# Optimization experiments

Measured on AMD Instinct MI355X. Metric: run time of the kernel, lower is better.

## Reference

```python
import jax, jax.numpy as jnp
import numpy as np

IM_H = 256.0
IM_W = 256.0


def setup_inputs() -> dict:
    key = jax.random.key(0)
    k1, k2 = jax.random.split(key)
    feats = jax.random.normal(k1, (8, 64, 64, 64), dtype=jnp.float32)
    Kcam = jax.random.normal(k2, (2, 4, 3, 4), dtype=jnp.float32)
    vmax = jnp.ones((2, 3), dtype=jnp.float32)
    vmin = jnp.zeros((2, 3), dtype=jnp.float32)
    return {"feats": feats, "Kcam": Kcam, "vmax": vmax, "vmin": vmin, "nvox": 48}


def reference(feats, Kcam, vmax, vmin, nvox):
    nR, fdim, fh, fw = feats.shape
    batch, view = Kcam.shape[0], Kcam.shape[1]
    rsz_h = float(fh) / IM_H
    rsz_w = float(fw) / IM_W

    # Build voxel grid per batch: linspace(vmin, vmax, nvox) along each axis.
    t = jnp.linspace(0.0, 1.0, nvox, dtype=jnp.float32)  # [nvox]
    rng = vmin[:, :, None] + (vmax - vmin)[:, :, None] * t  # [batch, 3, nvox]
    shp = (batch, nvox, nvox, nvox)
    gx = jnp.broadcast_to(rng[:, 0, :, None, None], shp)  # meshgrid 'ij' (torch default)
    gy = jnp.broadcast_to(rng[:, 1, None, :, None], shp)
    gz = jnp.broadcast_to(rng[:, 2, None, None, :], shp)
    grid = jnp.stack([gx, gy, gz], axis=1).reshape(batch, 3, -1)  # [batch, 3, nV]
    nV = grid.shape[2]
    rs_grid = jnp.concatenate([grid, jnp.ones((batch, 1, nV), jnp.float32)], axis=1)  # [batch, 4, nV]

    # Perspective projection: [batch, view*3, 4] @ [batch, 4, nV]
    im_p = jnp.einsum('bvrk,bkn->bvrn', Kcam, rs_grid).reshape(batch * view, 3, nV)
    im_x, im_y, im_z = im_p[:, 0, :], im_p[:, 1, :], im_p[:, 2, :]
    im_x = jnp.clip(im_x / im_z * rsz_w, 0.0, fw - 1)
    im_y = jnp.clip(im_y / im_z * rsz_h, 0.0, fh - 1)

    im_x0 = jnp.floor(im_x)
    im_x1 = jnp.clip(im_x0 + 1.0, 0.0, fw - 1)
    im_y0 = jnp.floor(im_y)
    im_y1 = jnp.clip(im_y0 + 1.0, 0.0, fh - 1)

    flat = feats.reshape(nR, fdim, fh * fw)  # [nR, fdim, fh*fw]

    def gather(xi, yi):
        idx = (yi * fw + xi).astype(jnp.int32)  # [nR, nV]
        return jax.vmap(lambda f, i: f[:, i])(flat, idx)  # [nR, fdim, nV]

    Ia = gather(im_x0, im_y0)
    Ib = gather(im_x0, im_y1)
    Ic = gather(im_x1, im_y0)
    Id = gather(im_x1, im_y1)

    wa = ((im_x1 - im_x) * (im_y1 - im_y))[:, None, :]
    wb = ((im_x1 - im_x) * (im_y - im_y0))[:, None, :]
    wc = ((im_x - im_x0) * (im_y1 - im_y))[:, None, :]
    wd = ((im_x - im_x0) * (im_y - im_y0))[:, None, :]

    Ibilin = wa * Ia + wb * Ib + wc * Ic + wd * Id  # [nR, fdim, nV]
    return Ibilin.reshape(nR, fdim, nvox, nvox, nvox)
```

## Files before the change

### kernel.cpp

```cpp
#include <hip/hip_runtime.h>


#define NR    8
#define FDIM  64
#define FH    64
#define FW    64
#define IMG   (FH * FW)
#define NVOX  48
#define NV    (NVOX * NVOX * NVOX)
#define THREADS 256
#define QUARTERS 4
#define VPB   (NV / QUARTERS)
#define ITERS (VPB / THREADS)
#define ROWS  64
#define RS    66

typedef float f32x4 __attribute__((ext_vector_type(4)));
typedef float f32x2 __attribute__((ext_vector_type(2)));

__device__ __forceinline__ int swz(int y, int x) {
    const int g = ((x >> 2) ^ (y & 15));
    return y * RS + (g << 2) + (x & 3);
}

__global__ __launch_bounds__(THREADS, 4) void proj_splat_kernel(
    const float* __restrict__ feats,
    const float* __restrict__ Kcam,
    const float* __restrict__ vmax,
    const float* __restrict__ vmin,
    float* __restrict__ out)
{
    __shared__ f32x2 lds2[ROWS * RS];

    const int t  = threadIdx.x;
    const int cp = blockIdx.x;
    const int qq = blockIdx.y;
    const int r  = blockIdx.z;
    const int b  = r >> 2;

    const float* c0 = feats + ((size_t)r * FDIM + 2 * cp) * IMG;
    const float* c1 = c0 + IMG;
    float* ldsf = reinterpret_cast<float*>(lds2);
#pragma unroll
    for (int p = 0; p < 4; ++p) {
        const int i = p * 1024 + t * 4;
        const int y = i >> 6;
        const int x = i & 63;
        const f32x4 a = *reinterpret_cast<const f32x4*>(c0 + i);
        const f32x4 bb = *reinterpret_cast<const f32x4*>(c1 + i);
        const int fb = 2 * swz(y, x);
        f32x4 s0 = { a.x, bb.x, a.y, bb.y };
        f32x4 s1 = { a.z, bb.z, a.w, bb.w };
        *reinterpret_cast<f32x4*>(ldsf + fb)     = s0;
        *reinterpret_cast<f32x4*>(ldsf + fb + 4) = s1;
    }
    __syncthreads();

    const float inv = 1.0f / (float)(NVOX - 1);
    const float* vmn = vmin + b * 3;
    const float* vmx = vmax + b * 3;
    const float ax = (vmx[0] - vmn[0]) * inv;
    const float ay = (vmx[1] - vmn[1]) * inv;
    const float az = (vmx[2] - vmn[2]) * inv;
    const float* K = Kcam + r * 12;
    const float A0 = K[0] * ax, B0 = K[1] * ay, D0 = K[2]  * az;
    const float C0 = K[0] * vmn[0] + K[1] * vmn[1] + K[2]  * vmn[2] + K[3];
    const float A1 = K[4] * ax, B1 = K[5] * ay, D1 = K[6]  * az;
    const float C1 = K[4] * vmn[0] + K[5] * vmn[1] + K[6]  * vmn[2] + K[7];
    const float A2 = K[8] * ax, B2 = K[9] * ay, D2 = K[10] * az;
    const float C2 = K[8] * vmn[0] + K[9] * vmn[1] + K[10] * vmn[2] + K[11];

    float* o0 = out + ((size_t)r * FDIM + 2 * cp) * NV;
    float* o1 = o0 + NV;

    int n = qq * VPB + t;
    int i = n / (NVOX * NVOX);
    int j = (n / NVOX) % NVOX;
    int k = n % NVOX;

    for (int it = 0; it < ITERS; ++it) {
        const float fi = (float)i, fj = (float)j, fk = (float)k;
        const float px = C0 + A0 * fi + B0 * fj + D0 * fk;
        const float py = C1 + A1 * fi + B1 * fj + D1 * fk;
        const float pz = C2 + A2 * fi + B2 * fj + D2 * fk;

        const float rz = 0.25f / pz;
        float imx = px * rz;
        float imy = py * rz;
        imx = fminf(fmaxf(imx, 0.0f), (float)(FW - 1));
        imy = fminf(fmaxf(imy, 0.0f), (float)(FH - 1));

        const float x0 = floorf(imx);
        const float x1 = fminf(x0 + 1.0f, (float)(FW - 1));
        const float y0 = floorf(imy);
        const float y1 = fminf(y0 + 1.0f, (float)(FH - 1));

        const float wa = (x1 - imx) * (y1 - imy);
        const float wc = (imx - x0) * (y1 - imy);
        const float wb = (x1 - imx) * (imy - y0);
        const float wd = (imx - x0) * (imy - y0);

        const int ix0 = (int)x0, ix1 = (int)x1;
        const int iy0 = (int)y0, iy1 = (int)y1;

        const f32x2 p00 = lds2[swz(iy0, ix0)];
        const f32x2 p01 = lds2[swz(iy0, ix1)];
        const f32x2 p10 = lds2[swz(iy1, ix0)];
        const f32x2 p11 = lds2[swz(iy1, ix1)];

        const float res0 = wa * p00.x + wc * p01.x + wb * p10.x + wd * p11.x;
        const float res1 = wa * p00.y + wc * p01.y + wb * p10.y + wd * p11.y;
        __builtin_nontemporal_store(res0, o0 + n);
        __builtin_nontemporal_store(res1, o1 + n);

        n += THREADS;
        k += 16;
        if (k >= NVOX) { k -= NVOX; j += 6; } else { j += 5; }
        if (j >= NVOX) { j -= NVOX; i += 1; }
    }
}

extern "C" void kernel_launch(void* const* d_in, const int* in_sizes, int n_in,
                              void* d_out, int out_size, void* d_ws, size_t ws_size,
                              hipStream_t stream) {
    const float* feats = (const float*)d_in[0];
    const float* Kcam  = (const float*)d_in[1];
    const float* vmax  = (const float*)d_in[2];
    const float* vmin  = (const float*)d_in[3];
    float* out = (float*)d_out;

    dim3 grid(FDIM / 2, QUARTERS, NR);
    dim3 block(THREADS);
    proj_splat_kernel<<<grid, block, 0, stream>>>(feats, Kcam, vmax, vmin, out);
}
```

Baseline: 254.6 us.

## Store features as fp16 in LDS, process two voxels per thread, split grid into octants

Feature tiles are converted to half2 and kept in shared memory with an XOR swizzle, which halves the LDS footprint so more blocks fit per CU (launch bounds raised to 8). Each thread now handles two adjacent voxels, advancing the projection incrementally, and writes them with a 2-wide vector store instead of nontemporal scalar stores. The reciprocal becomes a fast approximate rcp, and the grid is split into 8 voxel chunks instead of 4. The fp16 storage and approximate reciprocal reduce numerical precision and may exceed the output tolerance.

```diff
diff --git a/kernel.cpp b/kernel.cpp
--- a/kernel.cpp
+++ b/kernel.cpp
@@ -1,4 +1,5 @@
 #include <hip/hip_runtime.h>
+#include <hip/hip_fp16.h>
 
 
 #define NR    8
@@ -9,50 +10,43 @@
 #define NVOX  48
 #define NV    (NVOX * NVOX * NVOX)
 #define THREADS 256
-#define QUARTERS 4
-#define VPB   (NV / QUARTERS)
-#define ITERS (VPB / THREADS)
-#define ROWS  64
-#define RS    66
+#define OCTS  8
+#define VPB   (NV / OCTS)
+#define ITERS (VPB / (THREADS * 2))
 
 typedef float f32x4 __attribute__((ext_vector_type(4)));
 typedef float f32x2 __attribute__((ext_vector_type(2)));
 
-__device__ __forceinline__ int swz(int y, int x) {
-    const int g = ((x >> 2) ^ (y & 15));
-    return y * RS + (g << 2) + (x & 3);
+__device__ __forceinline__ int slotof(int y, int x) {
+    return (y << 6) + (x ^ (y & 31));
 }
 
-__global__ __launch_bounds__(THREADS, 4) void proj_splat_kernel(
+__global__ __launch_bounds__(THREADS, 8) void proj_splat_kernel(
     const float* __restrict__ feats,
     const float* __restrict__ Kcam,
     const float* __restrict__ vmax,
     const float* __restrict__ vmin,
     float* __restrict__ out)
 {
-    __shared__ f32x2 lds2[ROWS * RS];
+    __shared__ __half2 ldsh[IMG];
 
-    const int t  = threadIdx.x;
-    const int cp = blockIdx.x;
-    const int qq = blockIdx.y;
-    const int r  = blockIdx.z;
-    const int b  = r >> 2;
+    const int t   = threadIdx.x;
+    const int cp  = blockIdx.x;
+    const int oct = blockIdx.y;
+    const int r   = blockIdx.z;
+    const int b   = r >> 2;
 
     const float* c0 = feats + ((size_t)r * FDIM + 2 * cp) * IMG;
     const float* c1 = c0 + IMG;
-    float* ldsf = reinterpret_cast<float*>(lds2);
 #pragma unroll
-    for (int p = 0; p < 4; ++p) {
-        const int i = p * 1024 + t * 4;
-        const int y = i >> 6;
-        const int x = i & 63;
-        const f32x4 a = *reinterpret_cast<const f32x4*>(c0 + i);
-        const f32x4 bb = *reinterpret_cast<const f32x4*>(c1 + i);
-        const int fb = 2 * swz(y, x);
-        f32x4 s0 = { a.x, bb.x, a.y, bb.y };
-        f32x4 s1 = { a.z, bb.z, a.w, bb.w };
-        *reinterpret_cast<f32x4*>(ldsf + fb)     = s0;
-        *reinterpret_cast<f32x4*>(ldsf + fb + 4) = s1;
+    for (int q = 0; q < 4; ++q) {
+        const int idx = q * 1024 + t * 4;
+        const int y = idx >> 6, x = idx & 63;
+        const f32x4 a  = *reinterpret_cast<const f32x4*>(c0 + idx);
+        const f32x4 bb = *reinterpret_cast<const f32x4*>(c1 + idx);
+#pragma unroll
+        for (int m = 0; m < 4; ++m)
+            ldsh[slotof(y, x + m)] = __floats2half2_rn(a[m], bb[m]);
     }
     __syncthreads();
 
@@ -73,49 +67,58 @@
     float* o0 = out + ((size_t)r * FDIM + 2 * cp) * NV;
     float* o1 = o0 + NV;
 
-    int n = qq * VPB + t;
+    int n = oct * VPB + 2 * t;
     int i = n / (NVOX * NVOX);
     int j = (n / NVOX) % NVOX;
     int k = n % NVOX;
 
     for (int it = 0; it < ITERS; ++it) {
         const float fi = (float)i, fj = (float)j, fk = (float)k;
-        const float px = C0 + A0 * fi + B0 * fj + D0 * fk;
-        const float py = C1 + A1 * fi + B1 * fj + D1 * fk;
-        const float pz = C2 + A2 * fi + B2 * fj + D2 * fk;
+        float px = C0 + A0 * fi + B0 * fj + D0 * fk;
+        float py = C1 + A1 * fi + B1 * fj + D1 * fk;
+        float pz = C2 + A2 * fi + B2 * fj + D2 * fk;
 
-        const float rz = 0.25f / pz;
-        float imx = px * rz;
-        float imy = py * rz;
-        imx = fminf(fmaxf(imx, 0.0f), (float)(FW - 1));
-        imy = fminf(fmaxf(imy, 0.0f), (float)(FH - 1));
+        float r0[2], r1[2];
+#pragma unroll
+        for (int v = 0; v < 2; ++v) {
+            const float rz = __builtin_amdgcn_rcpf(pz) * 0.25f;
+            float imx = px * rz;
+            float imy = py * rz;
+            imx = fminf(fmaxf(imx, 0.0f), (float)(FW - 1));
+            imy = fminf(fmaxf(imy, 0.0f), (float)(FH - 1));
 
-        const float x0 = floorf(imx);
-        const float x1 = fminf(x0 + 1.0f, (float)(FW - 1));
-        const float y0 = floorf(imy);
-        const float y1 = fminf(y0 + 1.0f, (float)(FH - 1));
+            const float x0 = floorf(imx);
+            const float x1 = fminf(x0 + 1.0f, (float)(FW - 1));
+            const float y0 = floorf(imy);
+            const float y1 = fminf(y0 + 1.0f, (float)(FH - 1));
 
-        const float wa = (x1 - imx) * (y1 - imy);
-        const float wc = (imx - x0) * (y1 - imy);
-        const float wb = (x1 - imx) * (imy - y0);
-        const float wd = (imx - x0) * (imy - y0);
+            const float wa = (x1 - imx) * (y1 - imy);
+            const float wc = (imx - x0) * (y1 - imy);
+            const float wb = (x1 - imx) * (imy - y0);
+            const float wd = (imx - x0) * (imy - y0);
 
-        const int ix0 = (int)x0, ix1 = (int)x1;
-        const int iy0 = (int)y0, iy1 = (int)y1;
+            const int ix0 = (int)x0, ix1 = (int)x1;
+            const int iy0 = (int)y0, iy1 = (int)y1;
 
-        const f32x2 p00 = lds2[swz(iy0, ix0)];
-        const f32x2 p01 = lds2[swz(iy0, ix1)];
-        const f32x2 p10 = lds2[swz(iy1, ix0)];
-        const f32x2 p11 = lds2[swz(iy1, ix1)];
+            const float2 p00 = __half22float2(ldsh[slotof(iy0, ix0)]);
+            const float2 p01 = __half22float2(ldsh[slotof(iy0, ix1)]);
+            const float2 p10 = __half22float2(ldsh[slotof(iy1, ix0)]);
+            const float2 p11 = __half22float2(ldsh[slotof(iy1, ix1)]);
 
-        const float res0 = wa * p00.x + wc * p01.x + wb * p10.x + wd * p11.x;
-        const float res1 = wa * p00.y + wc * p01.y + wb * p10.y + wd * p11.y;
-        __builtin_nontemporal_store(res0, o0 + n);
-        __builtin_nontemporal_store(res1, o1 + n);
+            r0[v] = wa * p00.x + wc * p01.x + wb * p10.x + wd * p11.x;
+            r1[v] = wa * p00.y + wc * p01.y + wb * p10.y + wd * p11.y;
 
-        n += THREADS;
-        k += 16;
-        if (k >= NVOX) { k -= NVOX; j += 6; } else { j += 5; }
+            px += D0; py += D1; pz += D2;
+        }
+
+        const f32x2 w0 = { r0[0], r0[1] };
+        const f32x2 w1 = { r1[0], r1[1] };
+        *reinterpret_cast<f32x2*>(o0 + n) = w0;
+        *reinterpret_cast<f32x2*>(o1 + n) = w1;
+
+        n += 2 * THREADS;
+        k += 32;
+        if (k >= NVOX) { k -= NVOX; j += 11; } else { j += 10; }
         if (j >= NVOX) { j -= NVOX; i += 1; }
     }
 }
@@ -129,7 +132,7 @@
     const float* vmin  = (const float*)d_in[3];
     float* out = (float*)d_out;
 
-    dim3 grid(FDIM / 2, QUARTERS, NR);
+    dim3 grid(FDIM / 2, OCTS, NR);
     dim3 block(THREADS);
     proj_splat_kernel<<<grid, block, 0, stream>>>(feats, Kcam, vmax, vmin, out);
 }
```

Result: faster. 234.3 us (-8.0%).
